# Performance work log

Measured on AMD Instinct MI355X. Metric: run time of the kernel, lower is better.

## Reference

```python
import jax, jax.numpy as jnp
import numpy as np

HIDDEN = 2048
N_HEADS = 16
N_KV_HEADS = 8
HEAD_DIM = 128
MROPE_SECTION = [8, 8, 24, 24]          # sums to HEAD_DIM // 2
ROPE_THETA = 10000.0
B, S, CTX = 4, 1024, 2048
# per-frequency section index (which of the 4 position streams drives each freq)
_SEC_IDX = np.repeat(np.arange(len(MROPE_SECTION)), MROPE_SECTION)  # (HEAD_DIM//2,)


def setup_inputs() -> dict:
    key = jax.random.key(0)
    ks = jax.random.split(key, 6)
    return {
        "hidden_states": jax.random.normal(ks[0], (B, S, HIDDEN), jnp.float32),
        "Wqkv": jax.random.normal(ks[1], (HIDDEN, (N_HEADS + 2 * N_KV_HEADS) * HEAD_DIM), jnp.float32) * 0.02,
        "Wo": jax.random.normal(ks[2], (N_HEADS * HEAD_DIM, HIDDEN), jnp.float32) * 0.02,
        "ctx_k": jax.random.normal(ks[3], (B, CTX, N_KV_HEADS, HEAD_DIM), jnp.float32),
        "ctx_v": jax.random.normal(ks[4], (B, CTX, N_KV_HEADS, HEAD_DIM), jnp.float32),
        "position_ids": jax.random.randint(ks[5], (len(MROPE_SECTION), S), 0, CTX + S, jnp.int32),
    }


def _mrope_cos_sin(position_ids):
    # position_ids: (n_sections, S) int -> cos/sin of shape (S, HEAD_DIM)
    half = HEAD_DIM // 2
    inv_freq = 1.0 / (ROPE_THETA ** (jnp.arange(0, half, dtype=jnp.float32) * 2.0 / HEAD_DIM))
    freqs = position_ids.astype(jnp.float32)[:, :, None] * inv_freq[None, None, :]  # (4, S, half)
    sec = jnp.asarray(_SEC_IDX)[None, None, :]                                       # (1, 1, half)
    f = jnp.take_along_axis(freqs, jnp.broadcast_to(sec, (1,) + freqs.shape[1:]), axis=0)[0]  # (S, half)
    emb = jnp.concatenate([f, f], axis=-1)  # (S, HEAD_DIM)
    return jnp.cos(emb), jnp.sin(emb)


def _rotate_half(x):
    h = x.shape[-1] // 2
    return jnp.concatenate([-x[..., h:], x[..., :h]], axis=-1)


def reference(hidden_states, Wqkv, Wo, ctx_k, ctx_v, position_ids):
    b, s, _ = hidden_states.shape
    q_size = N_HEADS * HEAD_DIM
    kv_size = N_KV_HEADS * HEAD_DIM
    qkv = hidden_states @ Wqkv  # (B, S, q+2kv)
    q = qkv[..., :q_size].reshape(b, s, N_HEADS, HEAD_DIM)
    k = qkv[..., q_size:q_size + kv_size].reshape(b, s, N_KV_HEADS, HEAD_DIM)
    v = qkv[..., q_size + kv_size:].reshape(b, s, N_KV_HEADS, HEAD_DIM)

    cos, sin = _mrope_cos_sin(position_ids)        # (S, D) each
    cos = cos[None, :, None, :]
    sin = sin[None, :, None, :]
    q = q * cos + _rotate_half(q) * sin
    k = k * cos + _rotate_half(k) * sin

    # KV-cache concat along sequence dim
    k = jnp.concatenate([ctx_k, k], axis=1)        # (B, CTX+S, KV, D)
    v = jnp.concatenate([ctx_v, v], axis=1)

    # GQA: expand kv heads to query heads
    rep = N_HEADS // N_KV_HEADS
    k = jnp.repeat(k, rep, axis=2)                 # (B, T, H, D)
    v = jnp.repeat(v, rep, axis=2)

    scale = HEAD_DIM ** -0.5
    scores = jnp.einsum("bqhd,bkhd->bhqk", q, k) * scale  # non-causal
    probs = jax.nn.softmax(scores, axis=-1)
    out = jnp.einsum("bhqk,bkhd->bqhd", probs, v)  # (B, S, H, D)
    out = out.reshape(b, s, N_HEADS * HEAD_DIM)
    return out @ Wo
```

## Files before the change

kernel.cpp:

```cpp
#include <hip/hip_runtime.h>
#include <hip/hip_bf16.h>
#include <stdint.h>

#define NH 16
#define NKV 8
#define HD 128
#define BB 4
#define SS 1024
#define CTXL 2048
#define LT 3072
#define HID 2048
#define QKVN 4096
#define MROWS 4096

typedef __hip_bfloat16 bf16;
using f32x4 = __attribute__((ext_vector_type(4))) float;
using s16x8 = __attribute__((ext_vector_type(8))) short;

#define MFMA(a, b, c) __builtin_amdgcn_mfma_f32_16x16x32_bf16((a), (b), (c), 0, 0, 0)

__device__ __forceinline__ void gload_lds16(const void* g, void* l) {
  __builtin_amdgcn_global_load_lds((const __attribute__((address_space(1))) void*)g,
                                   (__attribute__((address_space(3))) void*)l, 16, 0, 0);
}

__device__ __forceinline__ void store_bf8(bf16* dst, const float* f) {
  bf16 tmp[8];
#pragma unroll
  for (int j = 0; j < 8; ++j) tmp[j] = __float2bfloat16(f[j]);
  __builtin_memcpy((void*)dst, (const void*)tmp, 16);
}


__global__ void cvt_bf16(const float* __restrict__ in, bf16* __restrict__ out) {
  size_t tid = (size_t)blockIdx.x * 256 + threadIdx.x;
  const float4* p = (const float4*)(in + tid * 8);
  float4 a = p[0], b = p[1];
  float f[8] = {a.x, a.y, a.z, a.w, b.x, b.y, b.z, b.w};
  store_bf8(out + tid * 8, f);
}

__global__ void transpose_cvt(const float* __restrict__ in, bf16* __restrict__ out,
                              int R, int C) {
  __shared__ float tile[32][33];
  int c0 = blockIdx.x * 32, r0 = blockIdx.y * 32;
  int tx = threadIdx.x & 31, ty = threadIdx.x >> 5;
#pragma unroll
  for (int i = 0; i < 32; i += 8)
    tile[ty + i][tx] = in[(size_t)(r0 + ty + i) * C + c0 + tx];
  __syncthreads();
#pragma unroll
  for (int i = 0; i < 32; i += 8)
    out[(size_t)(c0 + ty + i) * R + r0 + tx] = __float2bfloat16(tile[tx][ty + i]);
}

__global__ void ctxk_copy(const float* __restrict__ ck, bf16* __restrict__ Kf) {
  int tid = blockIdx.x * 256 + threadIdx.x;
  int d8 = tid & 15, l = (tid >> 4) & 2047, h = (tid >> 15) & 7, b = tid >> 18;
  const float* s = ck + (((size_t)b * CTXL + l) * NKV + h) * HD + d8 * 8;
  const float4* p = (const float4*)s;
  float4 a = p[0], bb = p[1];
  float f[8] = {a.x, a.y, a.z, a.w, bb.x, bb.y, bb.z, bb.w};
  store_bf8(Kf + (((size_t)(b * NKV + h)) * LT + l) * HD + d8 * 8, f);
}

__global__ void ctxv_transpose(const float* __restrict__ cv, bf16* __restrict__ Vt) {
  __shared__ float tile[32][33];
  int l0 = blockIdx.x * 32, d0 = blockIdx.y * 32;
  int b = blockIdx.z >> 3, h = blockIdx.z & 7;
  int tx = threadIdx.x & 31, ty = threadIdx.x >> 5;
#pragma unroll
  for (int i = 0; i < 32; i += 8)
    tile[ty + i][tx] = cv[(((size_t)b * CTXL + l0 + ty + i) * NKV + h) * HD + d0 + tx];
  __syncthreads();
#pragma unroll
  for (int i = 0; i < 32; i += 8)
    Vt[(((size_t)(b * NKV + h)) * HD + d0 + ty + i) * LT + l0 + tx] =
        __float2bfloat16(tile[tx][ty + i]);
}

__global__ void vt_from_qkv(const bf16* __restrict__ qkv, bf16* __restrict__ Vt) {
  __shared__ float tile[32][33];
  int s0 = blockIdx.x * 32, d0 = blockIdx.y * 32;
  int b = blockIdx.z >> 3, h = blockIdx.z & 7;
  int tx = threadIdx.x & 31, ty = threadIdx.x >> 5;
#pragma unroll
  for (int i = 0; i < 32; i += 8)
    tile[ty + i][tx] = __bfloat162float(
        qkv[((size_t)b * SS + s0 + ty + i) * QKVN + 3072 + h * HD + d0 + tx]);
  __syncthreads();
#pragma unroll
  for (int i = 0; i < 32; i += 8)
    Vt[(((size_t)(b * NKV + h)) * HD + d0 + ty + i) * LT + CTXL + s0 + tx] =
        __float2bfloat16(tile[tx][ty + i]);
}

__global__ void rope_table(const int* __restrict__ pid, float* __restrict__ cosT,
                           float* __restrict__ sinT) {
  int tid = blockIdx.x * 256 + threadIdx.x;
  int j = tid & 63, s = tid >> 6;
  int sec = (j < 8) ? 0 : (j < 16) ? 1 : (j < 40) ? 2 : 3;
  float pos = (float)pid[sec * SS + s];
  float inv = __expf(-(float)j * 0.14391156831212787f);
  float a = pos * inv;
  cosT[tid] = cosf(a);
  sinT[tid] = sinf(a);
}

__global__ void rope_q(const bf16* __restrict__ qkv, const float* __restrict__ cosT,
                       const float* __restrict__ sinT, bf16* __restrict__ Q) {
  int tid = blockIdx.x * 256 + threadIdx.x;
  int j = tid & 63, h = (tid >> 6) & 15, s = (tid >> 10) & 1023, b = tid >> 20;
  const bf16* src = qkv + ((size_t)b * SS + s) * QKVN + h * HD;
  float x1 = __bfloat162float(src[j]), x2 = __bfloat162float(src[j + 64]);
  float c = cosT[s * 64 + j], sn = sinT[s * 64 + j];
  bf16* dst = Q + (((size_t)(b * NH + h)) * SS + s) * HD;
  dst[j] = __float2bfloat16(x1 * c - x2 * sn);
  dst[j + 64] = __float2bfloat16(x2 * c + x1 * sn);
}

__global__ void rope_k(const bf16* __restrict__ qkv, const float* __restrict__ cosT,
                       const float* __restrict__ sinT, bf16* __restrict__ Kf) {
  int tid = blockIdx.x * 256 + threadIdx.x;
  int j = tid & 63, h = (tid >> 6) & 7, s = (tid >> 9) & 1023, b = tid >> 19;
  const bf16* src = qkv + ((size_t)b * SS + s) * QKVN + 2048 + h * HD;
  float x1 = __bfloat162float(src[j]), x2 = __bfloat162float(src[j + 64]);
  float c = cosT[s * 64 + j], sn = sinT[s * 64 + j];
  bf16* dst = Kf + (((size_t)(b * NKV + h)) * LT + CTXL + s) * HD;
  dst[j] = __float2bfloat16(x1 * c - x2 * sn);
  dst[j + 64] = __float2bfloat16(x2 * c + x1 * sn);
}


template <typename OT>
__global__ __launch_bounds__(512, 1) void gemm_bt(const bf16* __restrict__ A,
                                                  const bf16* __restrict__ BT,
                                                  OT* __restrict__ C, int M, int N,
                                                  int K) {
  __shared__ __attribute__((aligned(16))) bf16 lA[3][256][64];
  __shared__ __attribute__((aligned(16))) bf16 lB[3][128][64];
  const int t = threadIdx.x;
  const int lane = t & 63, w = t >> 6;
  const int wr = w >> 1, wc = w & 1;
  const int lrow = lane & 15, kgrp = lane >> 4;
  const int rchk = lrow & 7;
  const int lin = blockIdx.y * gridDim.x + blockIdx.x;
  const int qq = (gridDim.x * gridDim.y) >> 3;
  const int swz = (lin & 7) * qq + (lin >> 3);
  const int bx = swz % gridDim.x, by = swz / gridDim.x;
  const int m0 = by * 256, n0 = bx * 128;
  const int srow = lane >> 3;
  const int schk = (lane & 7) ^ srow;
  const f32x4 fz = {0.f, 0.f, 0.f, 0.f};
  f32x4 acc[4][4];
#pragma unroll
  for (int i = 0; i < 4; ++i)
#pragma unroll
    for (int j = 0; j < 4; ++j) acc[i][j] = fz;
  const int NTK = K >> 6;

#define GSTAGE(ib, kt)                                                      \
  do {                                                                      \
    _Pragma("unroll") for (int c = 0; c < 4; ++c) {                         \
      int ra = c * 64 + w * 8 + srow;                                       \
      gload_lds16(A + (size_t)(m0 + ra) * K + (kt)*64 + schk * 8,           \
                  &lA[ib][c * 64 + w * 8][0]);                              \
    }                                                                       \
    _Pragma("unroll") for (int c = 0; c < 2; ++c) {                         \
      int rb = c * 64 + w * 8 + srow;                                       \
      gload_lds16(BT + (size_t)(n0 + rb) * K + (kt)*64 + schk * 8,          \
                  &lB[ib][c * 64 + w * 8][0]);                              \
    }                                                                       \
  } while (0)

  GSTAGE(0, 0);
  GSTAGE(1, 1);
  int ib = 0;
  for (int kt = 0; kt < NTK; ++kt) {
    if (kt + 1 < NTK)
      asm volatile("s_waitcnt vmcnt(6) lgkmcnt(0)" ::: "memory");
    else
      asm volatile("s_waitcnt vmcnt(0) lgkmcnt(0)" ::: "memory");
    __builtin_amdgcn_s_barrier();
    __builtin_amdgcn_sched_barrier(0);
    if (kt + 2 < NTK) {
      int ib2 = ib + 2;
      if (ib2 >= 3) ib2 -= 3;
      GSTAGE(ib2, kt + 2);
    }
#pragma unroll
    for (int kk = 0; kk < 2; ++kk) {
      s16x8 af[4], bf[4];
#pragma unroll
      for (int i = 0; i < 4; ++i)
        af[i] = *(const s16x8*)&lA[ib][wr * 64 + i * 16 + lrow]
                                     [(((kk << 2) + kgrp) ^ rchk) * 8];
#pragma unroll
      for (int j = 0; j < 4; ++j)
        bf[j] = *(const s16x8*)&lB[ib][wc * 64 + j * 16 + lrow]
                                     [(((kk << 2) + kgrp) ^ rchk) * 8];
      __builtin_amdgcn_s_setprio(1);
#pragma unroll
      for (int i = 0; i < 4; ++i)
#pragma unroll
        for (int j = 0; j < 4; ++j) acc[i][j] = MFMA(af[i], bf[j], acc[i][j]);
      __builtin_amdgcn_s_setprio(0);
    }
    ++ib;
    if (ib >= 3) ib = 0;
  }
#undef GSTAGE

#pragma unroll
  for (int i = 0; i < 4; ++i)
#pragma unroll
    for (int j = 0; j < 4; ++j)
#pragma unroll
      for (int r = 0; r < 4; ++r) {
        int row = m0 + wr * 64 + i * 16 + kgrp * 4 + r;
        int col = n0 + wc * 64 + j * 16 + lrow;
        float v = acc[i][j][r];
        if constexpr (sizeof(OT) == 2)
          C[(size_t)row * N + col] = __float2bfloat16(v);
        else
          C[(size_t)row * N + col] = v;
      }
}


#define PSTR 72
#define NT 48
#define SCALE2 0.1275174335919605f

__global__ __launch_bounds__(512, 2) void flash_attn(
    const bf16* __restrict__ Q, const bf16* __restrict__ Kf,
    const bf16* __restrict__ Vt, bf16* __restrict__ O) {
  __shared__ __attribute__((aligned(16))) bf16 Kl[2][64][128];
  __shared__ __attribute__((aligned(16))) bf16 Vl[2][128][64];
  __shared__ __attribute__((aligned(16))) bf16 P_lds[8][32][PSTR];
  const int t = threadIdx.x, lane = t & 63, w = t >> 6;
  const int qb = blockIdx.x & 3, h = (blockIdx.x >> 2) & 15, b = blockIdx.x >> 6;
  const int hk = h >> 1;
  const int lrow = lane & 15, kgrp = lane >> 4;
  const bf16* Kp = Kf + (size_t)(b * NKV + hk) * LT * HD;
  const bf16* Vp = Vt + (size_t)(b * NKV + hk) * HD * LT;

  const bf16* Qp = Q + (((size_t)(b * NH + h)) * SS + qb * 256 + w * 32) * HD;
  s16x8 qf[2][4];
#pragma unroll
  for (int f = 0; f < 2; ++f)
#pragma unroll
    for (int kd = 0; kd < 4; ++kd)
      qf[f][kd] = *(const s16x8*)&Qp[(f * 16 + lrow) * HD + kd * 32 + kgrp * 8];

  const f32x4 fz = {0.f, 0.f, 0.f, 0.f};
  f32x4 acc[2][8];
#pragma unroll
  for (int f = 0; f < 2; ++f)
#pragma unroll
    for (int i = 0; i < 8; ++i) acc[f][i] = fz;
  float m_[2] = {-1e30f, -1e30f}, l_[2] = {0.f, 0.f};

#define STAGE_K(buf, l0)                                                        \
  do {                                                                          \
    _Pragma("unroll") for (int c = 0; c < 2; ++c) {                             \
      int row = w * 8 + c * 4 + (lane >> 4);                                    \
      gload_lds16(Kp + (size_t)((l0) + row) * HD + ((lane & 15) ^ (row & 15)) * 8, \
                  &Kl[buf][w * 8 + c * 4][0]);                                  \
    }                                                                           \
  } while (0)
#define STAGE_V(buf, l0)                                                        \
  do {                                                                          \
    _Pragma("unroll") for (int c = 0; c < 2; ++c) {                             \
      int d = w * 16 + c * 8 + (lane >> 3);                                     \
      gload_lds16(Vp + (size_t)d * LT + (l0) + ((lane & 7) ^ (d & 7)) * 8,      \
                  &Vl[buf][w * 16 + c * 8][0]);                                 \
    }                                                                           \
  } while (0)

  STAGE_K(0, 0);
  STAGE_V(0, 0);
  __syncthreads();

  for (int tt = 0; tt < NT; ++tt) {
    const int cur = tt & 1;
    if (tt + 1 < NT) {
      STAGE_K(cur ^ 1, (tt + 1) * 64);
      STAGE_V(cur ^ 1, (tt + 1) * 64);
    }

    f32x4 sc[2][4];
#pragma unroll
    for (int f = 0; f < 2; ++f)
#pragma unroll
      for (int cf = 0; cf < 4; ++cf) sc[f][cf] = fz;
    __builtin_amdgcn_s_setprio(1);
#pragma unroll
    for (int cf = 0; cf < 4; ++cf)
#pragma unroll
      for (int kd = 0; kd < 4; ++kd) {
        s16x8 kb =
            *(const s16x8*)&Kl[cur][cf * 16 + lrow][((kd * 4 + kgrp) ^ lrow) * 8];
#pragma unroll
        for (int f = 0; f < 2; ++f) sc[f][cf] = MFMA(kb, qf[f][kd], sc[f][cf]);
      }
    __builtin_amdgcn_s_setprio(0);

    float mxv[2];
#pragma unroll
    for (int f = 0; f < 2; ++f) {
      float a0 = fmaxf(fmaxf(sc[f][0][0], sc[f][0][1]),
                       fmaxf(sc[f][0][2], sc[f][0][3]));
      float a1 = fmaxf(fmaxf(sc[f][1][0], sc[f][1][1]),
                       fmaxf(sc[f][1][2], sc[f][1][3]));
      float a2 = fmaxf(fmaxf(sc[f][2][0], sc[f][2][1]),
                       fmaxf(sc[f][2][2], sc[f][2][3]));
      float a3 = fmaxf(fmaxf(sc[f][3][0], sc[f][3][1]),
                       fmaxf(sc[f][3][2], sc[f][3][3]));
      float mx = fmaxf(fmaxf(a0, a1), fmaxf(a2, a3)) * SCALE2;
      mx = fmaxf(mx, __shfl_xor(mx, 16, 64));
      mx = fmaxf(mx, __shfl_xor(mx, 32, 64));
      mxv[f] = mx;
    }
    bool nb = (mxv[0] > m_[0] + 8.f) || (mxv[1] > m_[1] + 8.f);
    if (__any(nb)) {
#pragma unroll
      for (int f = 0; f < 2; ++f) {
        float mn = fmaxf(m_[f], mxv[f]);
        float so = exp2f(m_[f] - mn);
        m_[f] = mn;
        l_[f] *= so;
        float sob[4];
#pragma unroll
        for (int r = 0; r < 4; ++r) sob[r] = __shfl(so, kgrp * 4 + r, 16);
#pragma unroll
        for (int nd = 0; nd < 8; ++nd)
#pragma unroll
          for (int r = 0; r < 4; ++r) acc[f][nd][r] *= sob[r];
      }
    }
#pragma unroll
    for (int f = 0; f < 2; ++f) {
      float lp = 0.f;
#pragma unroll
      for (int cf = 0; cf < 4; ++cf) {
        bf16 pk[4];
#pragma unroll
        for (int r = 0; r < 4; ++r) {
          float p = exp2f(sc[f][cf][r] * SCALE2 - m_[f]);
          lp += p;
          pk[r] = __float2bfloat16(p);
        }
        __builtin_memcpy((void*)&P_lds[w][f * 16 + lrow][cf * 16 + kgrp * 4], pk, 8);
      }
      l_[f] += lp;
    }

    s16x8 pa[2][2];
#pragma unroll
    for (int f = 0; f < 2; ++f)
#pragma unroll
      for (int kc = 0; kc < 2; ++kc)
        pa[f][kc] = *(const s16x8*)&P_lds[w][f * 16 + lrow][kc * 32 + kgrp * 8];

    __builtin_amdgcn_s_setprio(1);
#pragma unroll
    for (int nd = 0; nd < 8; ++nd)
#pragma unroll
      for (int kc = 0; kc < 2; ++kc) {
        s16x8 vb = *(const s16x8*)&Vl[cur][nd * 16 + lrow]
                                     [((kc * 4 + kgrp) ^ (lrow & 7)) * 8];
#pragma unroll
        for (int f = 0; f < 2; ++f) acc[f][nd] = MFMA(pa[f][kc], vb, acc[f][nd]);
      }
    __builtin_amdgcn_s_setprio(0);
    __syncthreads();
  }
#undef STAGE_K
#undef STAGE_V

  float li[2][4];
#pragma unroll
  for (int f = 0; f < 2; ++f) {
    float lv = l_[f];
    lv += __shfl_xor(lv, 16, 64);
    lv += __shfl_xor(lv, 32, 64);
#pragma unroll
    for (int r = 0; r < 4; ++r) li[f][r] = 1.f / __shfl(lv, kgrp * 4 + r, 16);
  }
#pragma unroll
  for (int f = 0; f < 2; ++f)
#pragma unroll
    for (int nd = 0; nd < 8; ++nd)
#pragma unroll
      for (int r = 0; r < 4; ++r) {
        int row = qb * 256 + w * 32 + f * 16 + kgrp * 4 + r;
        O[((size_t)b * SS + row) * 2048 + h * HD + nd * 16 + lrow] =
            __float2bfloat16(acc[f][nd][r] * li[f][r]);
      }
}


extern "C" void kernel_launch(void* const* d_in, const int* in_sizes, int n_in,
                              void* d_out, int out_size, void* d_ws, size_t ws_size,
                              hipStream_t stream) {
  const float* hs = (const float*)d_in[0];
  const float* Wqkv = (const float*)d_in[1];
  const float* Wo = (const float*)d_in[2];
  const float* ctx_k = (const float*)d_in[3];
  const float* ctx_v = (const float*)d_in[4];
  const int* pid = (const int*)d_in[5];
  float* out = (float*)d_out;
  char* ws = (char*)d_ws;

  bf16* Hb = (bf16*)(ws);
  bf16* WqT = (bf16*)(ws + 16777216);
  bf16* WoT = (bf16*)(ws + 33554432);
  bf16* qkv = (bf16*)(ws + 41943040);
  bf16* Qb = (bf16*)(ws + 75497472);
  bf16* Kfull = (bf16*)(ws + 92274688);
  bf16* Vt = (bf16*)(ws + 117440512);
  float* cosT = (float*)(ws + 142606336);
  float* sinT = (float*)(ws + 142606336 + 262144);
  bf16* attn = Hb;

  rope_table<<<256, 256, 0, stream>>>(pid, cosT, sinT);
  cvt_bf16<<<4096, 256, 0, stream>>>(hs, Hb);
  transpose_cvt<<<dim3(128, 64), 256, 0, stream>>>(Wqkv, WqT, HID, QKVN);
  transpose_cvt<<<dim3(64, 64), 256, 0, stream>>>(Wo, WoT, 2048, 2048);
  ctxk_copy<<<4096, 256, 0, stream>>>(ctx_k, Kfull);
  ctxv_transpose<<<dim3(64, 4, 32), 256, 0, stream>>>(ctx_v, Vt);
  gemm_bt<bf16><<<dim3(QKVN / 128, MROWS / 256), 512, 0, stream>>>(
      Hb, WqT, qkv, MROWS, QKVN, HID);
  rope_q<<<16384, 256, 0, stream>>>(qkv, cosT, sinT, Qb);
  rope_k<<<8192, 256, 0, stream>>>(qkv, cosT, sinT, Kfull);
  vt_from_qkv<<<dim3(32, 4, 32), 256, 0, stream>>>(qkv, Vt);
  flash_attn<<<256, 512, 0, stream>>>(Qb, Kfull, Vt, attn);
  gemm_bt<float><<<dim3(2048 / 128, MROWS / 256), 512, 0, stream>>>(
      attn, WoT, out, MROWS, 2048, HID);
}
```

Baseline: 357.8 us.

## Switch flash attention to 32x32x16 MFMA with register-resident P via lane shuffles

Rewrites the attention inner loop to use 32x32x16 bf16 MFMA tiles instead of 16x16x32. Each wave now handles its 32 query rows as one tile. The softmax probabilities are packed to bf16 and rearranged across half-waves with shuffles instead of being written to and read back from LDS, which removes the P_lds buffer and its LDS traffic. Launch bounds drop from 2 to 1 blocks per CU, which gives more registers per thread but may reduce occupancy and latency hiding. The s_setprio hints are also removed.

```diff
diff --git a/kernel.cpp b/kernel.cpp
--- a/kernel.cpp
+++ b/kernel.cpp
@@ -15,9 +15,12 @@
 
 typedef __hip_bfloat16 bf16;
 using f32x4 = __attribute__((ext_vector_type(4))) float;
+using f32x16 = __attribute__((ext_vector_type(16))) float;
 using s16x8 = __attribute__((ext_vector_type(8))) short;
+using u32x4 = __attribute__((ext_vector_type(4))) unsigned int;
 
 #define MFMA(a, b, c) __builtin_amdgcn_mfma_f32_16x16x32_bf16((a), (b), (c), 0, 0, 0)
+#define MFMA32(a, b, c) __builtin_amdgcn_mfma_f32_32x32x16_bf16((a), (b), (c), 0, 0, 0)
 
 __device__ __forceinline__ void gload_lds16(const void* g, void* l) {
   __builtin_amdgcn_global_load_lds((const __attribute__((address_space(1))) void*)g,
@@ -29,6 +32,14 @@
 #pragma unroll
   for (int j = 0; j < 8; ++j) tmp[j] = __float2bfloat16(f[j]);
   __builtin_memcpy((void*)dst, (const void*)tmp, 16);
+}
+
+__device__ __forceinline__ unsigned int pack_bf2(float lo, float hi) {
+  bf16 a = __float2bfloat16(lo), b = __float2bfloat16(hi);
+  unsigned short ua, ub;
+  __builtin_memcpy(&ua, &a, 2);
+  __builtin_memcpy(&ub, &b, 2);
+  return ((unsigned int)ub << 16) | ua;
 }
 
 
@@ -228,38 +239,33 @@
 }
 
 
-#define PSTR 72
 #define NT 48
 #define SCALE2 0.1275174335919605f
 
-__global__ __launch_bounds__(512, 2) void flash_attn(
+__global__ __launch_bounds__(512, 1) void flash_attn(
     const bf16* __restrict__ Q, const bf16* __restrict__ Kf,
     const bf16* __restrict__ Vt, bf16* __restrict__ O) {
   __shared__ __attribute__((aligned(16))) bf16 Kl[2][64][128];
   __shared__ __attribute__((aligned(16))) bf16 Vl[2][128][64];
-  __shared__ __attribute__((aligned(16))) bf16 P_lds[8][32][PSTR];
   const int t = threadIdx.x, lane = t & 63, w = t >> 6;
   const int qb = blockIdx.x & 3, h = (blockIdx.x >> 2) & 15, b = blockIdx.x >> 6;
   const int hk = h >> 1;
-  const int lrow = lane & 15, kgrp = lane >> 4;
+  const int l31 = lane & 31, hi = lane >> 5;
   const bf16* Kp = Kf + (size_t)(b * NKV + hk) * LT * HD;
   const bf16* Vp = Vt + (size_t)(b * NKV + hk) * HD * LT;
 
   const bf16* Qp = Q + (((size_t)(b * NH + h)) * SS + qb * 256 + w * 32) * HD;
-  s16x8 qf[2][4];
-#pragma unroll
-  for (int f = 0; f < 2; ++f)
-#pragma unroll
-    for (int kd = 0; kd < 4; ++kd)
-      qf[f][kd] = *(const s16x8*)&Qp[(f * 16 + lrow) * HD + kd * 32 + kgrp * 8];
-
-  const f32x4 fz = {0.f, 0.f, 0.f, 0.f};
-  f32x4 acc[2][8];
-#pragma unroll
-  for (int f = 0; f < 2; ++f)
-#pragma unroll
-    for (int i = 0; i < 8; ++i) acc[f][i] = fz;
-  float m_[2] = {-1e30f, -1e30f}, l_[2] = {0.f, 0.f};
+  s16x8 qf[8];
+#pragma unroll
+  for (int ds = 0; ds < 8; ++ds)
+    qf[ds] = *(const s16x8*)&Qp[l31 * HD + ds * 16 + hi * 8];
+
+  f32x16 acc[4];
+#pragma unroll
+  for (int dt = 0; dt < 4; ++dt)
+#pragma unroll
+    for (int r = 0; r < 16; ++r) acc[dt][r] = 0.f;
+  float m_ = -1e30f, l_ = 0.f;
 
 #define STAGE_K(buf, l0)                                                        \
   do {                                                                          \
@@ -289,115 +295,103 @@
       STAGE_V(cur ^ 1, (tt + 1) * 64);
     }
 
-    f32x4 sc[2][4];
-#pragma unroll
-    for (int f = 0; f < 2; ++f)
-#pragma unroll
-      for (int cf = 0; cf < 4; ++cf) sc[f][cf] = fz;
-    __builtin_amdgcn_s_setprio(1);
-#pragma unroll
-    for (int cf = 0; cf < 4; ++cf)
-#pragma unroll
-      for (int kd = 0; kd < 4; ++kd) {
-        s16x8 kb =
-            *(const s16x8*)&Kl[cur][cf * 16 + lrow][((kd * 4 + kgrp) ^ lrow) * 8];
-#pragma unroll
-        for (int f = 0; f < 2; ++f) sc[f][cf] = MFMA(kb, qf[f][kd], sc[f][cf]);
-      }
-    __builtin_amdgcn_s_setprio(0);
-
-    float mxv[2];
-#pragma unroll
-    for (int f = 0; f < 2; ++f) {
-      float a0 = fmaxf(fmaxf(sc[f][0][0], sc[f][0][1]),
-                       fmaxf(sc[f][0][2], sc[f][0][3]));
-      float a1 = fmaxf(fmaxf(sc[f][1][0], sc[f][1][1]),
-                       fmaxf(sc[f][1][2], sc[f][1][3]));
-      float a2 = fmaxf(fmaxf(sc[f][2][0], sc[f][2][1]),
-                       fmaxf(sc[f][2][2], sc[f][2][3]));
-      float a3 = fmaxf(fmaxf(sc[f][3][0], sc[f][3][1]),
-                       fmaxf(sc[f][3][2], sc[f][3][3]));
-      float mx = fmaxf(fmaxf(a0, a1), fmaxf(a2, a3)) * SCALE2;
-      mx = fmaxf(mx, __shfl_xor(mx, 16, 64));
-      mx = fmaxf(mx, __shfl_xor(mx, 32, 64));
-      mxv[f] = mx;
-    }
-    bool nb = (mxv[0] > m_[0] + 8.f) || (mxv[1] > m_[1] + 8.f);
-    if (__any(nb)) {
-#pragma unroll
-      for (int f = 0; f < 2; ++f) {
-        float mn = fmaxf(m_[f], mxv[f]);
-        float so = exp2f(m_[f] - mn);
-        m_[f] = mn;
-        l_[f] *= so;
-        float sob[4];
-#pragma unroll
-        for (int r = 0; r < 4; ++r) sob[r] = __shfl(so, kgrp * 4 + r, 16);
-#pragma unroll
-        for (int nd = 0; nd < 8; ++nd)
-#pragma unroll
-          for (int r = 0; r < 4; ++r) acc[f][nd][r] *= sob[r];
-      }
-    }
-#pragma unroll
-    for (int f = 0; f < 2; ++f) {
-      float lp = 0.f;
-#pragma unroll
-      for (int cf = 0; cf < 4; ++cf) {
-        bf16 pk[4];
-#pragma unroll
-        for (int r = 0; r < 4; ++r) {
-          float p = exp2f(sc[f][cf][r] * SCALE2 - m_[f]);
-          lp += p;
-          pk[r] = __float2bfloat16(p);
+    f32x16 sc0, sc1;
+#pragma unroll
+    for (int r = 0; r < 16; ++r) { sc0[r] = 0.f; sc1[r] = 0.f; }
+#pragma unroll
+    for (int ds = 0; ds < 8; ++ds) {
+      s16x8 k0 = *(const s16x8*)&Kl[cur][l31][((ds * 2 + hi) ^ (lane & 15)) * 8];
+      s16x8 k1 =
+          *(const s16x8*)&Kl[cur][32 + l31][((ds * 2 + hi) ^ (lane & 15)) * 8];
+      sc0 = MFMA32(k0, qf[ds], sc0);
+      sc1 = MFMA32(k1, qf[ds], sc1);
+    }
+
+    float mx = fmaxf(sc0[0], sc0[1]);
+#pragma unroll
+    for (int r = 2; r < 16; ++r) mx = fmaxf(mx, sc0[r]);
+#pragma unroll
+    for (int r = 0; r < 16; ++r) mx = fmaxf(mx, sc1[r]);
+    mx *= SCALE2;
+    mx = fmaxf(mx, __shfl_xor(mx, 32, 64));
+
+    if (__any(mx > m_ + 8.f)) {
+      float mn = fmaxf(m_, mx);
+      float so = exp2f(m_ - mn);
+      m_ = mn;
+      l_ *= so;
+      float sob[16];
+#pragma unroll
+      for (int r = 0; r < 16; ++r)
+        sob[r] = __shfl(so, (r & 3) + 8 * (r >> 2) + 4 * hi, 32);
+#pragma unroll
+      for (int dt = 0; dt < 4; ++dt)
+#pragma unroll
+        for (int r = 0; r < 16; ++r) acc[dt][r] *= sob[r];
+    }
+
+    float p0[16], p1[16], lp = 0.f;
+#pragma unroll
+    for (int r = 0; r < 16; ++r) {
+      p0[r] = exp2f(sc0[r] * SCALE2 - m_);
+      p1[r] = exp2f(sc1[r] * SCALE2 - m_);
+      lp += p0[r] + p1[r];
+    }
+    l_ += lp;
+    unsigned int w0[8], w1[8];
+#pragma unroll
+    for (int i = 0; i < 8; ++i) {
+      w0[i] = pack_bf2(p0[2 * i], p0[2 * i + 1]);
+      w1[i] = pack_bf2(p1[2 * i], p1[2 * i + 1]);
+    }
+    unsigned int x00 = __shfl_xor((int)(hi ? w0[0] : w0[2]), 32, 64);
+    unsigned int x01 = __shfl_xor((int)(hi ? w0[1] : w0[3]), 32, 64);
+    unsigned int x02 = __shfl_xor((int)(hi ? w0[4] : w0[6]), 32, 64);
+    unsigned int x03 = __shfl_xor((int)(hi ? w0[5] : w0[7]), 32, 64);
+    unsigned int x10 = __shfl_xor((int)(hi ? w1[0] : w1[2]), 32, 64);
+    unsigned int x11 = __shfl_xor((int)(hi ? w1[1] : w1[3]), 32, 64);
+    unsigned int x12 = __shfl_xor((int)(hi ? w1[4] : w1[6]), 32, 64);
+    unsigned int x13 = __shfl_xor((int)(hi ? w1[5] : w1[7]), 32, 64);
+    u32x4 pa[2][2];
+    pa[0][0] = u32x4{hi ? x00 : w0[0], hi ? x01 : w0[1],
+                     hi ? w0[2] : x00, hi ? w0[3] : x01};
+    pa[0][1] = u32x4{hi ? x02 : w0[4], hi ? x03 : w0[5],
+                     hi ? w0[6] : x02, hi ? w0[7] : x03};
+    pa[1][0] = u32x4{hi ? x10 : w1[0], hi ? x11 : w1[1],
+                     hi ? w1[2] : x10, hi ? w1[3] : x11};
+    pa[1][1] = u32x4{hi ? x12 : w1[4], hi ? x13 : w1[5],
+                     hi ? w1[6] : x12, hi ? w1[7] : x13};
+
+#pragma unroll
+    for (int dt = 0; dt < 4; ++dt) {
+#pragma unroll
+      for (int kt = 0; kt < 2; ++kt)
+#pragma unroll
+        for (int s = 0; s < 2; ++s) {
+          s16x8 vb = *(const s16x8*)&Vl[cur][dt * 32 + l31]
+                                       [((kt * 4 + s * 2 + hi) ^ (lane & 7)) * 8];
+          acc[dt] = MFMA32(__builtin_bit_cast(s16x8, pa[kt][s]), vb, acc[dt]);
         }
-        __builtin_memcpy((void*)&P_lds[w][f * 16 + lrow][cf * 16 + kgrp * 4], pk, 8);
-      }
-      l_[f] += lp;
-    }
-
-    s16x8 pa[2][2];
-#pragma unroll
-    for (int f = 0; f < 2; ++f)
-#pragma unroll
-      for (int kc = 0; kc < 2; ++kc)
-        pa[f][kc] = *(const s16x8*)&P_lds[w][f * 16 + lrow][kc * 32 + kgrp * 8];
-
-    __builtin_amdgcn_s_setprio(1);
-#pragma unroll
-    for (int nd = 0; nd < 8; ++nd)
-#pragma unroll
-      for (int kc = 0; kc < 2; ++kc) {
-        s16x8 vb = *(const s16x8*)&Vl[cur][nd * 16 + lrow]
-                                     [((kc * 4 + kgrp) ^ (lrow & 7)) * 8];
-#pragma unroll
-        for (int f = 0; f < 2; ++f) acc[f][nd] = MFMA(pa[f][kc], vb, acc[f][nd]);
-      }
-    __builtin_amdgcn_s_setprio(0);
+    }
     __syncthreads();
   }
 #undef STAGE_K
 #undef STAGE_V
 
-  float li[2][4];
-#pragma unroll
-  for (int f = 0; f < 2; ++f) {
-    float lv = l_[f];
-    lv += __shfl_xor(lv, 16, 64);
-    lv += __shfl_xor(lv, 32, 64);
-#pragma unroll
-    for (int r = 0; r < 4; ++r) li[f][r] = 1.f / __shfl(lv, kgrp * 4 + r, 16);
-  }
-#pragma unroll
-  for (int f = 0; f < 2; ++f)
-#pragma unroll
-    for (int nd = 0; nd < 8; ++nd)
-#pragma unroll
-      for (int r = 0; r < 4; ++r) {
-        int row = qb * 256 + w * 32 + f * 16 + kgrp * 4 + r;
-        O[((size_t)b * SS + row) * 2048 + h * HD + nd * 16 + lrow] =
-            __float2bfloat16(acc[f][nd][r] * li[f][r]);
-      }
+  float lv = l_ + __shfl_xor(l_, 32, 64);
+  float inv = 1.f / lv;
+  float li[16];
+#pragma unroll
+  for (int r = 0; r < 16; ++r)
+    li[r] = __shfl(inv, (r & 3) + 8 * (r >> 2) + 4 * hi, 32);
+#pragma unroll
+  for (int dt = 0; dt < 4; ++dt)
+#pragma unroll
+    for (int r = 0; r < 16; ++r) {
+      int row = qb * 256 + w * 32 + (r & 3) + 8 * (r >> 2) + 4 * hi;
+      O[((size_t)b * SS + row) * 2048 + h * HD + dt * 32 + l31] =
+          __float2bfloat16(acc[dt][r] * li[r]);
+    }
 }
 
 
```

Result: no change. 358.6 us (+0.2%).

## Merge prep kernels into two launches and fuse Q RoPE into attention

Applied to the files above, without the earlier changes.

The six preprocessing kernels become one block-indexed launch, and the K-RoPE and V-transpose kernels become a second. Query RoPE is now applied inside flash_attn, which reads Q straight from the qkv buffer with the cos/sin tables, so the separate Q buffer write and re-read go away. The s_setprio hints around the MFMA loops are also removed. This saves launch gaps and a round trip of Q through memory, at the cost of strided Q loads and a little extra register pressure in the attention prologue.

```diff
diff --git a/kernel.cpp b/kernel.cpp
--- a/kernel.cpp
+++ b/kernel.cpp
@@ -31,104 +31,120 @@
   __builtin_memcpy((void*)dst, (const void*)tmp, 16);
 }
 
-
-__global__ void cvt_bf16(const float* __restrict__ in, bf16* __restrict__ out) {
-  size_t tid = (size_t)blockIdx.x * 256 + threadIdx.x;
-  const float4* p = (const float4*)(in + tid * 8);
-  float4 a = p[0], b = p[1];
-  float f[8] = {a.x, a.y, a.z, a.w, b.x, b.y, b.z, b.w};
-  store_bf8(out + tid * 8, f);
-}
-
-__global__ void transpose_cvt(const float* __restrict__ in, bf16* __restrict__ out,
-                              int R, int C) {
+__device__ __forceinline__ float bf2f(short x) {
+  unsigned int u = ((unsigned int)(unsigned short)x) << 16;
+  float f;
+  __builtin_memcpy(&f, &u, 4);
+  return f;
+}
+
+#define P1_CVT 4096
+#define P1_WQ (P1_CVT + 8192)
+#define P1_WO (P1_WQ + 4096)
+#define P1_RT (P1_WO + 256)
+#define P1_CK (P1_RT + 4096)
+#define P1_CV (P1_CK + 8192)
+
+__global__ void prep1(const float* __restrict__ hs, const float* __restrict__ Wqkv,
+                      const float* __restrict__ Wo, const float* __restrict__ ck,
+                      const float* __restrict__ cv, const int* __restrict__ pid,
+                      bf16* __restrict__ Hb, bf16* __restrict__ WqT,
+                      bf16* __restrict__ WoT, bf16* __restrict__ Kf,
+                      bf16* __restrict__ Vt, float* __restrict__ cosT,
+                      float* __restrict__ sinT) {
   __shared__ float tile[32][33];
-  int c0 = blockIdx.x * 32, r0 = blockIdx.y * 32;
-  int tx = threadIdx.x & 31, ty = threadIdx.x >> 5;
-#pragma unroll
-  for (int i = 0; i < 32; i += 8)
-    tile[ty + i][tx] = in[(size_t)(r0 + ty + i) * C + c0 + tx];
-  __syncthreads();
-#pragma unroll
-  for (int i = 0; i < 32; i += 8)
-    out[(size_t)(c0 + ty + i) * R + r0 + tx] = __float2bfloat16(tile[tx][ty + i]);
-}
-
-__global__ void ctxk_copy(const float* __restrict__ ck, bf16* __restrict__ Kf) {
-  int tid = blockIdx.x * 256 + threadIdx.x;
-  int d8 = tid & 15, l = (tid >> 4) & 2047, h = (tid >> 15) & 7, b = tid >> 18;
-  const float* s = ck + (((size_t)b * CTXL + l) * NKV + h) * HD + d8 * 8;
-  const float4* p = (const float4*)s;
-  float4 a = p[0], bb = p[1];
-  float f[8] = {a.x, a.y, a.z, a.w, bb.x, bb.y, bb.z, bb.w};
-  store_bf8(Kf + (((size_t)(b * NKV + h)) * LT + l) * HD + d8 * 8, f);
-}
-
-__global__ void ctxv_transpose(const float* __restrict__ cv, bf16* __restrict__ Vt) {
+  const int blk = blockIdx.x, thr = threadIdx.x;
+  if (blk < P1_CVT) {
+    size_t tid = (size_t)blk * 256 + thr;
+    const float4* p = (const float4*)(hs + tid * 8);
+    float4 a = p[0], b = p[1];
+    float f[8] = {a.x, a.y, a.z, a.w, b.x, b.y, b.z, b.w};
+    store_bf8(Hb + tid * 8, f);
+  } else if (blk < P1_WQ) {
+    int j = blk - P1_CVT;
+    int c0 = (j & 127) * 32, r0 = (j >> 7) * 32;
+    int tx = thr & 31, ty = thr >> 5;
+#pragma unroll
+    for (int i = 0; i < 32; i += 8)
+      tile[ty + i][tx] = Wqkv[(size_t)(r0 + ty + i) * QKVN + c0 + tx];
+    __syncthreads();
+#pragma unroll
+    for (int i = 0; i < 32; i += 8)
+      WqT[(size_t)(c0 + ty + i) * HID + r0 + tx] = __float2bfloat16(tile[tx][ty + i]);
+  } else if (blk < P1_WO) {
+    int j = blk - P1_WQ;
+    int c0 = (j & 63) * 32, r0 = (j >> 6) * 32;
+    int tx = thr & 31, ty = thr >> 5;
+#pragma unroll
+    for (int i = 0; i < 32; i += 8)
+      tile[ty + i][tx] = Wo[(size_t)(r0 + ty + i) * 2048 + c0 + tx];
+    __syncthreads();
+#pragma unroll
+    for (int i = 0; i < 32; i += 8)
+      WoT[(size_t)(c0 + ty + i) * 2048 + r0 + tx] = __float2bfloat16(tile[tx][ty + i]);
+  } else if (blk < P1_RT) {
+    int tid = (blk - P1_WO) * 256 + thr;
+    int j = tid & 63, s = tid >> 6;
+    int sec = (j < 8) ? 0 : (j < 16) ? 1 : (j < 40) ? 2 : 3;
+    float pos = (float)pid[sec * SS + s];
+    float inv = __expf(-(float)j * 0.14391156831212787f);
+    float a = pos * inv;
+    cosT[tid] = cosf(a);
+    sinT[tid] = sinf(a);
+  } else if (blk < P1_CK) {
+    int tid = (blk - P1_RT) * 256 + thr;
+    int d8 = tid & 15, l = (tid >> 4) & 2047, h = (tid >> 15) & 7, b = tid >> 18;
+    const float* s = ck + (((size_t)b * CTXL + l) * NKV + h) * HD + d8 * 8;
+    const float4* p = (const float4*)s;
+    float4 a = p[0], bb = p[1];
+    float f[8] = {a.x, a.y, a.z, a.w, bb.x, bb.y, bb.z, bb.w};
+    store_bf8(Kf + (((size_t)(b * NKV + h)) * LT + l) * HD + d8 * 8, f);
+  } else {
+    int j = blk - P1_CK;
+    int l0 = (j & 63) * 32, d0 = ((j >> 6) & 3) * 32;
+    int bz = j >> 8, b = bz >> 3, h = bz & 7;
+    int tx = thr & 31, ty = thr >> 5;
+#pragma unroll
+    for (int i = 0; i < 32; i += 8)
+      tile[ty + i][tx] =
+          cv[(((size_t)b * CTXL + l0 + ty + i) * NKV + h) * HD + d0 + tx];
+    __syncthreads();
+#pragma unroll
+    for (int i = 0; i < 32; i += 8)
+      Vt[(((size_t)(b * NKV + h)) * HD + d0 + ty + i) * LT + l0 + tx] =
+          __float2bfloat16(tile[tx][ty + i]);
+  }
+}
+
+__global__ void prep2(const bf16* __restrict__ qkv, const float* __restrict__ cosT,
+                      const float* __restrict__ sinT, bf16* __restrict__ Kf,
+                      bf16* __restrict__ Vt) {
   __shared__ float tile[32][33];
-  int l0 = blockIdx.x * 32, d0 = blockIdx.y * 32;
-  int b = blockIdx.z >> 3, h = blockIdx.z & 7;
-  int tx = threadIdx.x & 31, ty = threadIdx.x >> 5;
-#pragma unroll
-  for (int i = 0; i < 32; i += 8)
-    tile[ty + i][tx] = cv[(((size_t)b * CTXL + l0 + ty + i) * NKV + h) * HD + d0 + tx];
-  __syncthreads();
-#pragma unroll
-  for (int i = 0; i < 32; i += 8)
-    Vt[(((size_t)(b * NKV + h)) * HD + d0 + ty + i) * LT + l0 + tx] =
-        __float2bfloat16(tile[tx][ty + i]);
-}
-
-__global__ void vt_from_qkv(const bf16* __restrict__ qkv, bf16* __restrict__ Vt) {
-  __shared__ float tile[32][33];
-  int s0 = blockIdx.x * 32, d0 = blockIdx.y * 32;
-  int b = blockIdx.z >> 3, h = blockIdx.z & 7;
-  int tx = threadIdx.x & 31, ty = threadIdx.x >> 5;
-#pragma unroll
-  for (int i = 0; i < 32; i += 8)
-    tile[ty + i][tx] = __bfloat162float(
-        qkv[((size_t)b * SS + s0 + ty + i) * QKVN + 3072 + h * HD + d0 + tx]);
-  __syncthreads();
-#pragma unroll
-  for (int i = 0; i < 32; i += 8)
-    Vt[(((size_t)(b * NKV + h)) * HD + d0 + ty + i) * LT + CTXL + s0 + tx] =
-        __float2bfloat16(tile[tx][ty + i]);
-}
-
-__global__ void rope_table(const int* __restrict__ pid, float* __restrict__ cosT,
-                           float* __restrict__ sinT) {
-  int tid = blockIdx.x * 256 + threadIdx.x;
-  int j = tid & 63, s = tid >> 6;
-  int sec = (j < 8) ? 0 : (j < 16) ? 1 : (j < 40) ? 2 : 3;
-  float pos = (float)pid[sec * SS + s];
-  float inv = __expf(-(float)j * 0.14391156831212787f);
-  float a = pos * inv;
-  cosT[tid] = cosf(a);
-  sinT[tid] = sinf(a);
-}
-
-__global__ void rope_q(const bf16* __restrict__ qkv, const float* __restrict__ cosT,
-                       const float* __restrict__ sinT, bf16* __restrict__ Q) {
-  int tid = blockIdx.x * 256 + threadIdx.x;
-  int j = tid & 63, h = (tid >> 6) & 15, s = (tid >> 10) & 1023, b = tid >> 20;
-  const bf16* src = qkv + ((size_t)b * SS + s) * QKVN + h * HD;
-  float x1 = __bfloat162float(src[j]), x2 = __bfloat162float(src[j + 64]);
-  float c = cosT[s * 64 + j], sn = sinT[s * 64 + j];
-  bf16* dst = Q + (((size_t)(b * NH + h)) * SS + s) * HD;
-  dst[j] = __float2bfloat16(x1 * c - x2 * sn);
-  dst[j + 64] = __float2bfloat16(x2 * c + x1 * sn);
-}
-
-__global__ void rope_k(const bf16* __restrict__ qkv, const float* __restrict__ cosT,
-                       const float* __restrict__ sinT, bf16* __restrict__ Kf) {
-  int tid = blockIdx.x * 256 + threadIdx.x;
-  int j = tid & 63, h = (tid >> 6) & 7, s = (tid >> 9) & 1023, b = tid >> 19;
-  const bf16* src = qkv + ((size_t)b * SS + s) * QKVN + 2048 + h * HD;
-  float x1 = __bfloat162float(src[j]), x2 = __bfloat162float(src[j + 64]);
-  float c = cosT[s * 64 + j], sn = sinT[s * 64 + j];
-  bf16* dst = Kf + (((size_t)(b * NKV + h)) * LT + CTXL + s) * HD;
-  dst[j] = __float2bfloat16(x1 * c - x2 * sn);
-  dst[j + 64] = __float2bfloat16(x2 * c + x1 * sn);
+  const int blk = blockIdx.x, thr = threadIdx.x;
+  if (blk < 8192) {
+    int tid = blk * 256 + thr;
+    int j = tid & 63, h = (tid >> 6) & 7, s = (tid >> 9) & 1023, b = tid >> 19;
+    const bf16* src = qkv + ((size_t)b * SS + s) * QKVN + 2048 + h * HD;
+    float x1 = __bfloat162float(src[j]), x2 = __bfloat162float(src[j + 64]);
+    float c = cosT[s * 64 + j], sn = sinT[s * 64 + j];
+    bf16* dst = Kf + (((size_t)(b * NKV + h)) * LT + CTXL + s) * HD;
+    dst[j] = __float2bfloat16(x1 * c - x2 * sn);
+    dst[j + 64] = __float2bfloat16(x2 * c + x1 * sn);
+  } else {
+    int j = blk - 8192;
+    int s0 = (j & 31) * 32, d0 = ((j >> 5) & 3) * 32;
+    int bz = j >> 7, b = bz >> 3, h = bz & 7;
+    int tx = thr & 31, ty = thr >> 5;
+#pragma unroll
+    for (int i = 0; i < 32; i += 8)
+      tile[ty + i][tx] = __bfloat162float(
+          qkv[((size_t)b * SS + s0 + ty + i) * QKVN + 3072 + h * HD + d0 + tx]);
+    __syncthreads();
+#pragma unroll
+    for (int i = 0; i < 32; i += 8)
+      Vt[(((size_t)(b * NKV + h)) * HD + d0 + ty + i) * LT + CTXL + s0 + tx] =
+          __float2bfloat16(tile[tx][ty + i]);
+  }
 }
 
 
@@ -233,7 +249,8 @@
 #define SCALE2 0.1275174335919605f
 
 __global__ __launch_bounds__(512, 2) void flash_attn(
-    const bf16* __restrict__ Q, const bf16* __restrict__ Kf,
+    const bf16* __restrict__ qkv, const float* __restrict__ cosT,
+    const float* __restrict__ sinT, const bf16* __restrict__ Kf,
     const bf16* __restrict__ Vt, bf16* __restrict__ O) {
   __shared__ __attribute__((aligned(16))) bf16 Kl[2][64][128];
   __shared__ __attribute__((aligned(16))) bf16 Vl[2][128][64];
@@ -245,13 +262,40 @@
   const bf16* Kp = Kf + (size_t)(b * NKV + hk) * LT * HD;
   const bf16* Vp = Vt + (size_t)(b * NKV + hk) * HD * LT;
 
-  const bf16* Qp = Q + (((size_t)(b * NH + h)) * SS + qb * 256 + w * 32) * HD;
   s16x8 qf[2][4];
 #pragma unroll
-  for (int f = 0; f < 2; ++f)
+  for (int f = 0; f < 2; ++f) {
+    int srw_i = qb * 256 + w * 32 + f * 16 + lrow;
+    const bf16* qrow = qkv + ((size_t)b * SS + srw_i) * QKVN + h * HD;
+    s16x8 qr[4];
 #pragma unroll
     for (int kd = 0; kd < 4; ++kd)
-      qf[f][kd] = *(const s16x8*)&Qp[(f * 16 + lrow) * HD + kd * 32 + kgrp * 8];
+      qr[kd] = *(const s16x8*)&qrow[kd * 32 + kgrp * 8];
+    const float* crow = cosT + srw_i * 64 + kgrp * 8;
+    const float* srow = sinT + srw_i * 64 + kgrp * 8;
+    float qv[4][8], cc[2][8], ssv[2][8];
+#pragma unroll
+    for (int kd = 0; kd < 4; ++kd)
+#pragma unroll
+      for (int j = 0; j < 8; ++j) qv[kd][j] = bf2f(qr[kd][j]);
+#pragma unroll
+    for (int g = 0; g < 2; ++g)
+#pragma unroll
+      for (int j = 0; j < 8; ++j) {
+        cc[g][j] = crow[g * 32 + j];
+        ssv[g][j] = srow[g * 32 + j];
+      }
+    bf16 o[4][8];
+#pragma unroll
+    for (int j = 0; j < 8; ++j) {
+      o[0][j] = __float2bfloat16(qv[0][j] * cc[0][j] - qv[2][j] * ssv[0][j]);
+      o[1][j] = __float2bfloat16(qv[1][j] * cc[1][j] - qv[3][j] * ssv[1][j]);
+      o[2][j] = __float2bfloat16(qv[2][j] * cc[0][j] + qv[0][j] * ssv[0][j]);
+      o[3][j] = __float2bfloat16(qv[3][j] * cc[1][j] + qv[1][j] * ssv[1][j]);
+    }
+#pragma unroll
+    for (int kd = 0; kd < 4; ++kd) __builtin_memcpy(&qf[f][kd], o[kd], 16);
+  }
 
   const f32x4 fz = {0.f, 0.f, 0.f, 0.f};
   f32x4 acc[2][8];
@@ -294,7 +338,6 @@
     for (int f = 0; f < 2; ++f)
 #pragma unroll
       for (int cf = 0; cf < 4; ++cf) sc[f][cf] = fz;
-    __builtin_amdgcn_s_setprio(1);
 #pragma unroll
     for (int cf = 0; cf < 4; ++cf)
 #pragma unroll
@@ -304,7 +347,6 @@
 #pragma unroll
         for (int f = 0; f < 2; ++f) sc[f][cf] = MFMA(kb, qf[f][kd], sc[f][cf]);
       }
-    __builtin_amdgcn_s_setprio(0);
 
     float mxv[2];
 #pragma unroll
@@ -363,7 +405,6 @@
       for (int kc = 0; kc < 2; ++kc)
         pa[f][kc] = *(const s16x8*)&P_lds[w][f * 16 + lrow][kc * 32 + kgrp * 8];
 
-    __builtin_amdgcn_s_setprio(1);
 #pragma unroll
     for (int nd = 0; nd < 8; ++nd)
 #pragma unroll
@@ -373,7 +414,6 @@
 #pragma unroll
         for (int f = 0; f < 2; ++f) acc[f][nd] = MFMA(pa[f][kc], vb, acc[f][nd]);
       }
-    __builtin_amdgcn_s_setprio(0);
     __syncthreads();
   }
 #undef STAGE_K
@@ -417,25 +457,18 @@
   bf16* WqT = (bf16*)(ws + 16777216);
   bf16* WoT = (bf16*)(ws + 33554432);
   bf16* qkv = (bf16*)(ws + 41943040);
-  bf16* Qb = (bf16*)(ws + 75497472);
   bf16* Kfull = (bf16*)(ws + 92274688);
   bf16* Vt = (bf16*)(ws + 117440512);
   float* cosT = (float*)(ws + 142606336);
   float* sinT = (float*)(ws + 142606336 + 262144);
   bf16* attn = Hb;
 
-  rope_table<<<256, 256, 0, stream>>>(pid, cosT, sinT);
-  cvt_bf16<<<4096, 256, 0, stream>>>(hs, Hb);
-  transpose_cvt<<<dim3(128, 64), 256, 0, stream>>>(Wqkv, WqT, HID, QKVN);
-  transpose_cvt<<<dim3(64, 64), 256, 0, stream>>>(Wo, WoT, 2048, 2048);
-  ctxk_copy<<<4096, 256, 0, stream>>>(ctx_k, Kfull);
-  ctxv_transpose<<<dim3(64, 4, 32), 256, 0, stream>>>(ctx_v, Vt);
+  prep1<<<P1_CV, 256, 0, stream>>>(hs, Wqkv, Wo, ctx_k, ctx_v, pid, Hb, WqT, WoT,
+                                   Kfull, Vt, cosT, sinT);
   gemm_bt<bf16><<<dim3(QKVN / 128, MROWS / 256), 512, 0, stream>>>(
       Hb, WqT, qkv, MROWS, QKVN, HID);
-  rope_q<<<16384, 256, 0, stream>>>(qkv, cosT, sinT, Qb);
-  rope_k<<<8192, 256, 0, stream>>>(qkv, cosT, sinT, Kfull);
-  vt_from_qkv<<<dim3(32, 4, 32), 256, 0, stream>>>(qkv, Vt);
-  flash_attn<<<256, 512, 0, stream>>>(Qb, Kfull, Vt, attn);
+  prep2<<<12288, 256, 0, stream>>>(qkv, cosT, sinT, Kfull, Vt);
+  flash_attn<<<256, 512, 0, stream>>>(qkv, cosT, sinT, Kfull, Vt, attn);
   gemm_bt<float><<<dim3(2048 / 128, MROWS / 256), 512, 0, stream>>>(
       attn, WoT, out, MROWS, 2048, HID);
 }
```

New measurement: 340.0 us. 1.05x faster.
